# Kernel optimization log

Measured on AMD Instinct MI355X. Metric: run time of the kernel, lower is better.

Reference implementation:

```python
import jax, jax.numpy as jnp
import numpy as np

N, F, T, HID, E = 50000, 8, 12, 64, 1600000


def setup_inputs() -> dict:
    key = jax.random.key(0)
    ks = jax.random.split(key, 9)
    x = jax.random.normal(ks[0], (N, F, T), jnp.float32)
    edge_index = jax.random.randint(ks[1], (2, E), 0, N)
    edge_weight = jax.random.uniform(ks[2], (E,), jnp.float32)
    # GCNConv weights for the z/r/h gates, fused along the output dim -> (F, 3*HID)
    s = 1.0 / np.sqrt(F)
    conv_w = jax.random.uniform(ks[3], (F, 3 * HID), jnp.float32, -s, s)
    conv_b = jnp.zeros((3 * HID,), jnp.float32)
    # TGCN gate linears: input is concat([conv_out, H]) of width 2*HID
    s2 = 1.0 / np.sqrt(2 * HID)
    lin_w = jax.random.uniform(ks[4], (3, 2 * HID, HID), jnp.float32, -s2, s2)
    lin_b = jax.random.uniform(ks[5], (3, HID), jnp.float32, -s2, s2)
    attention = jax.random.uniform(ks[6], (T,), jnp.float32)
    sc = 1.0 / np.sqrt(HID)
    cls_w = jax.random.uniform(ks[7], (HID, T), jnp.float32, -sc, sc)
    cls_b = jax.random.uniform(ks[8], (T,), jnp.float32, -sc, sc)
    return dict(x=x, edge_index=edge_index, edge_weight=edge_weight,
                conv_w=conv_w, conv_b=conv_b, lin_w=lin_w, lin_b=lin_b,
                attention=attention, cls_w=cls_w, cls_b=cls_b)


def _gcn_norm(edge_index, edge_weight, num_nodes):
    # PyG gcn_norm: add self-loops (weight 1), symmetric D^-1/2 (A+I) D^-1/2
    src, dst = edge_index[0], edge_index[1]
    loop = jnp.arange(num_nodes)
    src = jnp.concatenate([src, loop])
    dst = jnp.concatenate([dst, loop])
    w = jnp.concatenate([edge_weight, jnp.ones((num_nodes,), edge_weight.dtype)])
    deg = jax.ops.segment_sum(w, dst, num_segments=num_nodes)
    dinv = jnp.where(deg > 0, jax.lax.rsqrt(deg), 0.0)
    return src, dst, dinv[src] * w * dinv[dst]


def reference(x, edge_index, edge_weight, conv_w, conv_b, lin_w, lin_b, attention, cls_w, cls_b):
    num_nodes, _, periods = x.shape
    hid = cls_w.shape[0]
    src, dst, norm = _gcn_norm(edge_index, edge_weight, num_nodes)
    probs = jax.nn.softmax(attention)
    Hzero = jnp.zeros((num_nodes, hid), x.dtype)  # A3TGCN passes the same H (None->0) each period
    H_accum = jnp.zeros((num_nodes, hid), x.dtype)
    for t in range(periods):
        xw = x[:, :, t] @ conv_w  # (N, 3*hid)
        conv = jax.ops.segment_sum(xw[src] * norm[:, None], dst, num_segments=num_nodes) + conv_b
        cz, cr, ch = jnp.split(conv, 3, axis=1)
        Z = jax.nn.sigmoid(jnp.concatenate([cz, Hzero], axis=1) @ lin_w[0] + lin_b[0])
        R = jax.nn.sigmoid(jnp.concatenate([cr, Hzero], axis=1) @ lin_w[1] + lin_b[1])
        H_tilde = jnp.tanh(jnp.concatenate([ch, Hzero * R], axis=1) @ lin_w[2] + lin_b[2])
        H_new = Z * Hzero + (1.0 - Z) * H_tilde
        H_accum = H_accum + probs[t] * H_new
    h = jax.nn.relu(H_accum)
    return h @ cls_w + cls_b  # (N, periods)
```

## Files before the change

### kernel.cpp

```cpp
#include <hip/hip_runtime.h>
#include <hip/hip_fp16.h>
#include <math.h>

#define NN 50000
#define FD 8
#define TD 12
#define HD 64
#define FT 96
#define EE 1600000
#define NBUK 391
#define TILE 16384
#define NT 98
#define XB 586
#define SORTCAP 5120

#define OFF_GHIST 0
#define OFF_BASE  512
#define OFF_CUR   1024
#define OFF_ROWST 2048
#define OFF_DINV  (2048 + NN + 16)
#define OFF_FUSED (OFF_DINV + NN)
#define OFF_THIST (OFF_FUSED + 1184)
#define OFF_XH    (OFF_THIST + 38400)
#define OFF_BEDGE (OFF_XH + NN*48)
#define OFF_AGGH  (OFF_BEDGE + 2*EE)

__device__ inline void h8f(uint4 h, float* f) {
    const __half2* p = (const __half2*)&h;
#pragma unroll
    for (int i = 0; i < 4; ++i) {
        float2 v = __half22float2(p[i]);
        f[2 * i] = v.x; f[2 * i + 1] = v.y;
    }
}

__device__ inline uint4 f8h(const float* f) {
    uint4 o;
    __half2* p = (__half2*)&o;
#pragma unroll
    for (int i = 0; i < 4; ++i) p[i] = __floats2half2_rn(f[2 * i], f[2 * i + 1]);
    return o;
}

__global__ __launch_bounds__(1024) void k_front(const float* __restrict__ x,
                                                uint4* __restrict__ xh4,
                                                const int* __restrict__ ei,
                                                int* __restrict__ ghist,
                                                int* __restrict__ thist,
                                                const float* __restrict__ conv_w,
                                                const float* __restrict__ conv_b,
                                                const float* __restrict__ lin_w,
                                                const float* __restrict__ lin_b,
                                                const float* __restrict__ attention,
                                                float* __restrict__ fused) {
    int b = blockIdx.x;
    int tid = threadIdx.x;
    if (b < NT) {
        __shared__ int h[NBUK];
        for (int i = tid; i < NBUK; i += 1024) h[i] = 0;
        __syncthreads();
        int base = b * TILE;
        for (int i = 0; i < TILE / 1024; ++i) {
            int e = base + i * 1024 + tid;
            if (e < EE) atomicAdd(&h[ei[EE + e] >> 7], 1);
        }
        __syncthreads();
        int* trow = thist + b * NBUK;
        for (int i = tid; i < NBUK; i += 1024) {
            int c = h[i];
            trow[i] = c;
            if (c) atomicAdd(&ghist[i], c);
        }
    } else if (b < NT + XB) {
        unsigned i = (unsigned)(b - NT) * 1024u + tid;
        if (i < (unsigned)NN * 12u) {
            unsigned n = i / 12u, t = i - n * 12u;
            const float* xp = x + (size_t)n * FT + t;
            float f[8];
#pragma unroll
            for (int k = 0; k < 8; ++k) f[k] = xp[k * 12];
            xh4[i] = f8h(f);
        }
    } else {
        for (int idx = tid; idx < 1024; idx += 1024) {
            int sel = idx >> 9;
            int f = (idx & 511) >> 6;
            int h = idx & 63;
            const float* cw = conv_w + f * 192 + (sel ? 128 : 0);
            const float* lw = lin_w + (sel ? 2 * 128 * 64 : 0) + h;
            float s = 0.f;
            for (int k = 0; k < 64; ++k) s += cw[k] * lw[k * 64];
            fused[idx] = s;
        }
        if (tid < 128) {
            int sel = tid >> 6;
            int h = tid & 63;
            const float* cb = conv_b + (sel ? 128 : 0);
            const float* lw = lin_w + (sel ? 2 * 128 * 64 : 0) + h;
            float s = lin_b[(sel ? 2 * 64 : 0) + h];
            for (int k = 0; k < 64; ++k) s += cb[k] * lw[k * 64];
            fused[1024 + tid] = s;
        }
        if (tid == 0) {
            float m = attention[0];
            for (int t = 1; t < TD; ++t) m = fmaxf(m, attention[t]);
            float e[TD], sum = 0.f;
            for (int t = 0; t < TD; ++t) { e[t] = __expf(attention[t] - m); sum += e[t]; }
            for (int t = 0; t < TD; ++t) fused[1152 + t] = e[t] / sum;
        }
    }
}

__global__ void k_scan(const int* __restrict__ ghist, int* __restrict__ bktbase,
                       int* __restrict__ cursor) {
    __shared__ int s[512];
    int tid = threadIdx.x;
    int v = (tid < NBUK) ? ghist[tid] : 0;
    s[tid] = v;
    __syncthreads();
    for (int off = 1; off < 512; off <<= 1) {
        int t = (tid >= off) ? s[tid - off] : 0;
        __syncthreads();
        s[tid] += t;
        __syncthreads();
    }
    int excl = s[tid] - v;
    if (tid < NBUK) { bktbase[tid] = excl; cursor[tid] = excl; }
    if (tid == NBUK - 1) bktbase[NBUK] = excl + v;
}

__global__ __launch_bounds__(1024) void k_place(const int* __restrict__ ei,
                                                const float* __restrict__ w,
                                                const int* __restrict__ thist,
                                                int* __restrict__ cursor,
                                                int2* __restrict__ bedge) {
    __shared__ int h[NBUK], bbase[NBUK];
    int tid = threadIdx.x;
    const int* tcnt = thist + blockIdx.x * NBUK;
    for (int i = tid; i < NBUK; i += 1024) {
        int c = tcnt[i];
        bbase[i] = c ? atomicAdd(&cursor[i], c) : 0;
        h[i] = 0;
    }
    __syncthreads();
    int base = blockIdx.x * TILE;
    for (int i = 0; i < TILE / 1024; ++i) {
        int e = base + i * 1024 + tid;
        if (e < EE) {
            int dst = ei[EE + e];
            int bk = dst >> 7;
            int rank = atomicAdd(&h[bk], 1);
            bedge[bbase[bk] + rank] =
                make_int2(ei[e] | ((dst & 127) << 16), __float_as_int(w[e]));
        }
    }
}

__global__ __launch_bounds__(512) void k_sort(const int* __restrict__ bktbase,
                                              int2* __restrict__ bedge,
                                              int* __restrict__ rowstart,
                                              float* __restrict__ dinv) {
    __shared__ int2 stage[SORTCAP];
    __shared__ int cnt[128];
    __shared__ float wd[128];
    __shared__ int rowbase[128];
    int tid = threadIdx.x, b = blockIdx.x;
    int es = bktbase[b], ee = bktbase[b + 1];
    int count = ee - es;
    if (count > SORTCAP) count = SORTCAP;
    if (tid < 128) { cnt[tid] = 0; wd[tid] = 0.f; }
    __syncthreads();
    for (int i = tid; i < count; i += 512) {
        int2 u = bedge[es + i];
        stage[i] = u;
        int dl = u.x >> 16;
        atomicAdd(&cnt[dl], 1);
        atomicAdd(&wd[dl], __int_as_float(u.y));
    }
    __syncthreads();
    if (tid < 128) rowbase[tid] = cnt[tid];
    __syncthreads();
    for (int off = 1; off < 128; off <<= 1) {
        int t = 0;
        if (tid >= off && tid < 128) t = rowbase[tid - off];
        __syncthreads();
        if (tid < 128) rowbase[tid] += t;
        __syncthreads();
    }
    int dbase = b << 7;
    if (tid < 128) {
        int excl = rowbase[tid] - cnt[tid];
        rowbase[tid] = excl;
        if (dbase + tid < NN) {
            rowstart[dbase + tid] = es + excl;
            dinv[dbase + tid] = rsqrtf(1.0f + wd[tid]);
        }
        cnt[tid] = 0;
    }
    if (b == NBUK - 1 && tid == 0) rowstart[NN] = ee;
    __syncthreads();
    for (int i = tid; i < count; i += 512) {
        int2 u = stage[i];
        int dl = u.x >> 16;
        int pos = atomicAdd(&cnt[dl], 1);
        bedge[es + rowbase[dl] + pos] = make_int2(u.x & 0xFFFF, u.y);
    }
}

__global__ __launch_bounds__(256) void k_gather(const uint4* __restrict__ xh4,
                                                const float* __restrict__ dinv,
                                                const int* __restrict__ rowstart,
                                                const int2* __restrict__ edata,
                                                uint4* __restrict__ aggh) {
    unsigned t = blockIdx.x * 256u + threadIdx.x;
    if (t >= (unsigned)NN * 12u) return;
    unsigned n = t / 12u;
    unsigned c = t - n * 12u;
    float dv = dinv[n];
    float a[8];
    h8f(xh4[n * 12u + c], a);
#pragma unroll
    for (int j = 0; j < 8; ++j) a[j] *= dv;
    int rs = rowstart[n], re = rowstart[n + 1];
    int k = rs;
    for (; k + 3 < re; k += 4) {
        int2 p0 = edata[k], p1 = edata[k + 1], p2 = edata[k + 2], p3 = edata[k + 3];
        float c0 = dinv[p0.x] * __int_as_float(p0.y);
        float c1 = dinv[p1.x] * __int_as_float(p1.y);
        float c2 = dinv[p2.x] * __int_as_float(p2.y);
        float c3 = dinv[p3.x] * __int_as_float(p3.y);
        float v0[8], v1[8], v2[8], v3[8];
        h8f(xh4[(unsigned)p0.x * 12u + c], v0);
        h8f(xh4[(unsigned)p1.x * 12u + c], v1);
        h8f(xh4[(unsigned)p2.x * 12u + c], v2);
        h8f(xh4[(unsigned)p3.x * 12u + c], v3);
#pragma unroll
        for (int j = 0; j < 8; ++j)
            a[j] += c0 * v0[j] + c1 * v1[j] + c2 * v2[j] + c3 * v3[j];
    }
    for (; k < re; ++k) {
        int2 p = edata[k];
        float co = dinv[p.x] * __int_as_float(p.y);
        float v[8];
        h8f(xh4[(unsigned)p.x * 12u + c], v);
#pragma unroll
        for (int j = 0; j < 8; ++j) a[j] += co * v[j];
    }
#pragma unroll
    for (int j = 0; j < 8; ++j) a[j] *= dv;
    aggh[n * 12u + c] = f8h(a);
}

__global__ __launch_bounds__(256) void k_node(const uint4* __restrict__ aggh,
                                              const float* __restrict__ fused,
                                              const float* __restrict__ cls_w,
                                              const float* __restrict__ cls_b,
                                              float* __restrict__ out) {
    __shared__ float r_lds[32 * 100];
    __shared__ float rel_lds[32 * 68];
    __shared__ float cwT_lds[12 * 68];
    __shared__ float cb_lds[12];
    __shared__ float probs_lds[12];
    int tid = threadIdx.x;
    int nbase = blockIdx.x * 32;

    for (int id = tid; id < 384; id += 256) {
        int nl = id / 12, c = id - nl * 12;
        float f[8] = {0, 0, 0, 0, 0, 0, 0, 0};
        int n = nbase + nl;
        if (n < NN) h8f(aggh[(size_t)n * 12 + c], f);
        *(float4*)&r_lds[nl * 100 + c * 8] = make_float4(f[0], f[1], f[2], f[3]);
        *(float4*)&r_lds[nl * 100 + c * 8 + 4] = make_float4(f[4], f[5], f[6], f[7]);
    }
    for (int id = tid; id < 768; id += 256) {
        int hh = id / 12, t = id - hh * 12;
        cwT_lds[t * 68 + hh] = cls_w[id];
    }
    if (tid < 12) { cb_lds[tid] = cls_b[tid]; probs_lds[tid] = fused[1152 + tid]; }

    int h = tid & 63;
    int w = tid >> 6;
    float wz[FD], wh[FD];
#pragma unroll
    for (int f = 0; f < FD; ++f) {
        wz[f] = fused[f * 64 + h];
        wh[f] = fused[512 + f * 64 + h];
    }
    float bz = fused[1024 + h], bh = fused[1088 + h];
    __syncthreads();

#pragma unroll
    for (int np = 0; np < 4; ++np) {
        int nl0 = w * 8 + np * 2;
        const float* rp0 = &r_lds[nl0 * 100];
        const float* rp1 = rp0 + 100;
        float acc0 = 0.f, acc1 = 0.f;
#pragma unroll
        for (int t = 0; t < TD; ++t) {
            float4 a0 = *(const float4*)&rp0[t * 8];
            float4 a1 = *(const float4*)&rp0[t * 8 + 4];
            float4 b0 = *(const float4*)&rp1[t * 8];
            float4 b1 = *(const float4*)&rp1[t * 8 + 4];
            float z0 = bz, h0 = bh, z1 = bz, h1 = bh;
            z0 += a0.x * wz[0] + a0.y * wz[1] + a0.z * wz[2] + a0.w * wz[3]
                + a1.x * wz[4] + a1.y * wz[5] + a1.z * wz[6] + a1.w * wz[7];
            h0 += a0.x * wh[0] + a0.y * wh[1] + a0.z * wh[2] + a0.w * wh[3]
                + a1.x * wh[4] + a1.y * wh[5] + a1.z * wh[6] + a1.w * wh[7];
            z1 += b0.x * wz[0] + b0.y * wz[1] + b0.z * wz[2] + b0.w * wz[3]
                + b1.x * wz[4] + b1.y * wz[5] + b1.z * wz[6] + b1.w * wz[7];
            h1 += b0.x * wh[0] + b0.y * wh[1] + b0.z * wh[2] + b0.w * wh[3]
                + b1.x * wh[4] + b1.y * wh[5] + b1.z * wh[6] + b1.w * wh[7];
            float om0 = __builtin_amdgcn_rcpf(1.f + __expf(z0));
            float om1 = __builtin_amdgcn_rcpf(1.f + __expf(z1));
            float Ht0 = 1.f - 2.f * __builtin_amdgcn_rcpf(1.f + __expf(2.f * h0));
            float Ht1 = 1.f - 2.f * __builtin_amdgcn_rcpf(1.f + __expf(2.f * h1));
            float p = probs_lds[t];
            acc0 += p * om0 * Ht0;
            acc1 += p * om1 * Ht1;
        }
        rel_lds[nl0 * 68 + h] = fmaxf(acc0, 0.f);
        rel_lds[(nl0 + 1) * 68 + h] = fmaxf(acc1, 0.f);
    }
    __syncthreads();

    for (int id = tid; id < 384; id += 256) {
        int nl = id / 12, t = id - nl * 12;
        int n = nbase + nl;
        if (n >= NN) continue;
        const float* rl = &rel_lds[nl * 68];
        const float* cwr = &cwT_lds[t * 68];
        float s = cb_lds[t];
#pragma unroll
        for (int k = 0; k < 16; ++k) {
            float4 rv = *(const float4*)&rl[k * 4];
            float4 cv = *(const float4*)&cwr[k * 4];
            s += rv.x * cv.x + rv.y * cv.y + rv.z * cv.z + rv.w * cv.w;
        }
        out[(size_t)n * TD + t] = s;
    }
}

extern "C" void kernel_launch(void* const* d_in, const int* in_sizes, int n_in,
                              void* d_out, int out_size, void* d_ws, size_t ws_size,
                              hipStream_t stream) {
    const float* x         = (const float*)d_in[0];
    const int*   ei        = (const int*)d_in[1];
    const float* w         = (const float*)d_in[2];
    const float* conv_w    = (const float*)d_in[3];
    const float* conv_b    = (const float*)d_in[4];
    const float* lin_w     = (const float*)d_in[5];
    const float* lin_b     = (const float*)d_in[6];
    const float* attention = (const float*)d_in[7];
    const float* cls_w     = (const float*)d_in[8];
    const float* cls_b     = (const float*)d_in[9];
    float* ws  = (float*)d_ws;
    float* out = (float*)d_out;

    int*   ghist    = (int*)(ws + OFF_GHIST);
    int*   bktbase  = (int*)(ws + OFF_BASE);
    int*   cursor   = (int*)(ws + OFF_CUR);
    int*   rowstart = (int*)(ws + OFF_ROWST);
    float* dinv     = ws + OFF_DINV;
    float* fused    = ws + OFF_FUSED;
    int*   thist    = (int*)(ws + OFF_THIST);
    uint4* xh4      = (uint4*)(ws + OFF_XH);
    int2*  bedge    = (int2*)(ws + OFF_BEDGE);
    uint4* aggh     = (uint4*)(ws + OFF_AGGH);

    hipMemsetAsync(ghist, 0, NBUK * sizeof(int), stream);
    k_front<<<NT + XB + 1, 1024, 0, stream>>>(x, xh4, ei, ghist, thist,
                                              conv_w, conv_b, lin_w, lin_b,
                                              attention, fused);
    k_scan<<<1, 512, 0, stream>>>(ghist, bktbase, cursor);
    k_place<<<NT, 1024, 0, stream>>>(ei, w, thist, cursor, bedge);
    k_sort<<<NBUK, 512, 0, stream>>>(bktbase, bedge, rowstart, dinv);
    {
        unsigned total = (unsigned)NN * 12u;
        k_gather<<<(total + 255) / 256, 256, 0, stream>>>(xh4, dinv,
                                                          rowstart, bedge, aggh);
    }
    k_node<<<(NN + 31) / 32, 256, 0, stream>>>(aggh, fused, cls_w, cls_b, out);
}
```

Before: 158.2 us.

## Precompute per-edge src-dinv coefficients, unroll gather by 8, keep half-precision in LDS

Adds a k_coeff pass that folds dinv[src] into each sorted edge weight once, so the gather no longer does a dependent dinv lookup per edge for each of the 12 channel threads. The gather loop is unrolled to 8 edges, with all index and feature loads issued before the math to raise memory-level parallelism. k_node now keeps the aggregated half-precision rows in LDS and converts them at use, which shrinks its shared-memory footprint. The trade-offs are an extra kernel launch that reads and writes the 1.6M-entry edge array, and more registers in the gather.

```diff
diff --git a/kernel.cpp b/kernel.cpp
--- a/kernel.cpp
+++ b/kernel.cpp
@@ -207,6 +207,15 @@
     }
 }
 
+__global__ __launch_bounds__(256) void k_coeff(const float* __restrict__ dinv,
+                                               int2* __restrict__ bedge) {
+    int e = blockIdx.x * 256 + threadIdx.x;
+    if (e >= EE) return;
+    int2 p = bedge[e];
+    p.y = __float_as_int(dinv[p.x] * __int_as_float(p.y));
+    bedge[e] = p;
+}
+
 __global__ __launch_bounds__(256) void k_gather(const uint4* __restrict__ xh4,
                                                 const float* __restrict__ dinv,
                                                 const int* __restrict__ rowstart,
@@ -223,24 +232,25 @@
     for (int j = 0; j < 8; ++j) a[j] *= dv;
     int rs = rowstart[n], re = rowstart[n + 1];
     int k = rs;
-    for (; k + 3 < re; k += 4) {
-        int2 p0 = edata[k], p1 = edata[k + 1], p2 = edata[k + 2], p3 = edata[k + 3];
-        float c0 = dinv[p0.x] * __int_as_float(p0.y);
-        float c1 = dinv[p1.x] * __int_as_float(p1.y);
-        float c2 = dinv[p2.x] * __int_as_float(p2.y);
-        float c3 = dinv[p3.x] * __int_as_float(p3.y);
-        float v0[8], v1[8], v2[8], v3[8];
-        h8f(xh4[(unsigned)p0.x * 12u + c], v0);
-        h8f(xh4[(unsigned)p1.x * 12u + c], v1);
-        h8f(xh4[(unsigned)p2.x * 12u + c], v2);
-        h8f(xh4[(unsigned)p3.x * 12u + c], v3);
-#pragma unroll
-        for (int j = 0; j < 8; ++j)
-            a[j] += c0 * v0[j] + c1 * v1[j] + c2 * v2[j] + c3 * v3[j];
+    for (; k + 7 < re; k += 8) {
+        int2 p[8];
+#pragma unroll
+        for (int q = 0; q < 8; ++q) p[q] = edata[k + q];
+        uint4 hv[8];
+#pragma unroll
+        for (int q = 0; q < 8; ++q) hv[q] = xh4[(unsigned)p[q].x * 12u + c];
+#pragma unroll
+        for (int q = 0; q < 8; ++q) {
+            float v[8];
+            h8f(hv[q], v);
+            float co = __int_as_float(p[q].y);
+#pragma unroll
+            for (int j = 0; j < 8; ++j) a[j] += co * v[j];
+        }
     }
     for (; k < re; ++k) {
         int2 p = edata[k];
-        float co = dinv[p.x] * __int_as_float(p.y);
+        float co = __int_as_float(p.y);
         float v[8];
         h8f(xh4[(unsigned)p.x * 12u + c], v);
 #pragma unroll
@@ -256,7 +266,7 @@
                                               const float* __restrict__ cls_w,
                                               const float* __restrict__ cls_b,
                                               float* __restrict__ out) {
-    __shared__ float r_lds[32 * 100];
+    __shared__ uint4 r4_lds[32 * 12];
     __shared__ float rel_lds[32 * 68];
     __shared__ float cwT_lds[12 * 68];
     __shared__ float cb_lds[12];
@@ -266,11 +276,10 @@
 
     for (int id = tid; id < 384; id += 256) {
         int nl = id / 12, c = id - nl * 12;
-        float f[8] = {0, 0, 0, 0, 0, 0, 0, 0};
         int n = nbase + nl;
-        if (n < NN) h8f(aggh[(size_t)n * 12 + c], f);
-        *(float4*)&r_lds[nl * 100 + c * 8] = make_float4(f[0], f[1], f[2], f[3]);
-        *(float4*)&r_lds[nl * 100 + c * 8 + 4] = make_float4(f[4], f[5], f[6], f[7]);
+        uint4 v = make_uint4(0, 0, 0, 0);
+        if (n < NN) v = aggh[(size_t)n * 12 + c];
+        r4_lds[nl * 12 + c] = v;
     }
     for (int id = tid; id < 768; id += 256) {
         int hh = id / 12, t = id - hh * 12;
@@ -292,24 +301,22 @@
 #pragma unroll
     for (int np = 0; np < 4; ++np) {
         int nl0 = w * 8 + np * 2;
-        const float* rp0 = &r_lds[nl0 * 100];
-        const float* rp1 = rp0 + 100;
+        const uint4* rp0 = &r4_lds[nl0 * 12];
+        const uint4* rp1 = rp0 + 12;
         float acc0 = 0.f, acc1 = 0.f;
 #pragma unroll
         for (int t = 0; t < TD; ++t) {
-            float4 a0 = *(const float4*)&rp0[t * 8];
-            float4 a1 = *(const float4*)&rp0[t * 8 + 4];
-            float4 b0 = *(const float4*)&rp1[t * 8];
-            float4 b1 = *(const float4*)&rp1[t * 8 + 4];
+            float va[8], vb[8];
+            h8f(rp0[t], va);
+            h8f(rp1[t], vb);
             float z0 = bz, h0 = bh, z1 = bz, h1 = bh;
-            z0 += a0.x * wz[0] + a0.y * wz[1] + a0.z * wz[2] + a0.w * wz[3]
-                + a1.x * wz[4] + a1.y * wz[5] + a1.z * wz[6] + a1.w * wz[7];
-            h0 += a0.x * wh[0] + a0.y * wh[1] + a0.z * wh[2] + a0.w * wh[3]
-                + a1.x * wh[4] + a1.y * wh[5] + a1.z * wh[6] + a1.w * wh[7];
-            z1 += b0.x * wz[0] + b0.y * wz[1] + b0.z * wz[2] + b0.w * wz[3]
-                + b1.x * wz[4] + b1.y * wz[5] + b1.z * wz[6] + b1.w * wz[7];
-            h1 += b0.x * wh[0] + b0.y * wh[1] + b0.z * wh[2] + b0.w * wh[3]
-                + b1.x * wh[4] + b1.y * wh[5] + b1.z * wh[6] + b1.w * wh[7];
+#pragma unroll
+            for (int f = 0; f < FD; ++f) {
+                z0 += va[f] * wz[f];
+                h0 += va[f] * wh[f];
+                z1 += vb[f] * wz[f];
+                h1 += vb[f] * wh[f];
+            }
             float om0 = __builtin_amdgcn_rcpf(1.f + __expf(z0));
             float om1 = __builtin_amdgcn_rcpf(1.f + __expf(z1));
             float Ht0 = 1.f - 2.f * __builtin_amdgcn_rcpf(1.f + __expf(2.f * h0));
@@ -374,6 +381,7 @@
     k_scan<<<1, 512, 0, stream>>>(ghist, bktbase, cursor);
     k_place<<<NT, 1024, 0, stream>>>(ei, w, thist, cursor, bedge);
     k_sort<<<NBUK, 512, 0, stream>>>(bktbase, bedge, rowstart, dinv);
+    k_coeff<<<(EE + 255) / 256, 256, 0, stream>>>(dinv, bedge);
     {
         unsigned total = (unsigned)NN * 12u;
         k_gather<<<(total + 255) / 256, 256, 0, stream>>>(xh4, dinv,
```

New measurement: 175.2 us. +10.8%, slower.
